# Performance work log

Measured on AMD Instinct MI355X. Metric: run time of the kernel, lower is better.

## Reference

```python
import jax, jax.numpy as jnp
import numpy as np

NUM_HEADS = 8
LN_EPS = 1e-5


def _layernorm(t, w, b):
    mu = t.mean(-1, keepdims=True)
    var = t.var(-1, keepdims=True)  # ddof=0, matches torch LayerNorm
    return (t - mu) * jax.lax.rsqrt(var + LN_EPS) * w + b


def setup_inputs() -> dict:
    key = jax.random.key(0)
    ks = jax.random.split(key, 5)
    B, C, H, W = 16, 384, 32, 32
    hidden = 4 * C
    s = 0.02
    return {
        "x": jax.random.normal(ks[0], (B, C, H, W), jnp.float32),
        "ln1_w": jnp.ones((C,), jnp.float32),
        "ln1_b": jnp.zeros((C,), jnp.float32),
        "qkv_w": s * jax.random.normal(ks[1], (3 * C, C), jnp.float32),
        "qkv_b": jnp.zeros((3 * C,), jnp.float32),
        "proj_w": s * jax.random.normal(ks[2], (C, C), jnp.float32),
        "proj_b": jnp.zeros((C,), jnp.float32),
        "ln2_w": jnp.ones((C,), jnp.float32),
        "ln2_b": jnp.zeros((C,), jnp.float32),
        "fc1_w": s * jax.random.normal(ks[3], (hidden, C), jnp.float32),
        "fc1_b": jnp.zeros((hidden,), jnp.float32),
        "fc2_w": s * jax.random.normal(ks[4], (C, hidden), jnp.float32),
        "fc2_b": jnp.zeros((C,), jnp.float32),
    }


def reference(x, ln1_w, ln1_b, qkv_w, qkv_b, proj_w, proj_b,
              ln2_w, ln2_b, fc1_w, fc1_b, fc2_w, fc2_b):
    B, C, H, W = x.shape
    N = H * W
    nh = NUM_HEADS
    hd = C // nh
    scale = hd ** (-0.5)

    xf = x.reshape(B, C, N).transpose(0, 2, 1)  # (B, N, C) tokens

    # --- pre-norm attention ---
    h1 = _layernorm(xf, ln1_w, ln1_b)
    qkv = h1 @ qkv_w.T + qkv_b                      # (B, N, 3C)
    qkv = qkv.reshape(B, N, 3, nh, hd).transpose(2, 0, 3, 1, 4)  # (3,B,h,N,d)
    q, k, v = qkv[0], qkv[1], qkv[2]
    attn = jax.nn.softmax(jnp.einsum('bhnd,bhmd->bhnm', q, k) * scale, axis=-1)
    out = jnp.einsum('bhnm,bhmd->bhnd', attn, v)    # (B,h,N,d)
    out = out.transpose(0, 2, 1, 3).reshape(B, N, C)
    out = out @ proj_w.T + proj_b
    xf = xf + out

    # --- pre-norm FFN (exact GELU, matching torch nn.GELU default) ---
    h2 = _layernorm(xf, ln2_w, ln2_b)
    f = jax.nn.gelu(h2 @ fc1_w.T + fc1_b, approximate=False)
    f = f @ fc2_w.T + fc2_b
    xf = xf + f

    return xf.transpose(0, 2, 1).reshape(B, C, H, W)
```

## Files before the change

kernel.cpp:

```cpp
#include <hip/hip_runtime.h>

typedef unsigned short u16;
using bf16x8 = __attribute__((ext_vector_type(8))) short;
using f32x4  = __attribute__((ext_vector_type(4))) float;
using f32x16 = __attribute__((ext_vector_type(16))) float;

#define DEV __device__ __forceinline__

constexpr int    NTOK = 16384;
constexpr size_t QKSZ = (size_t)16 * 8 * 1024 * 64;
constexpr float  ATTN_SCALE = 0.14433756729740645f;

DEV u16 f2bf(float x) {
  unsigned int u = __float_as_uint(x);
  u += 0x7fffu + ((u >> 16) & 1u);
  return (u16)(u >> 16);
}

DEV void async16(const u16* g, u16* l) {
  __builtin_amdgcn_global_load_lds(
      (const __attribute__((address_space(1))) unsigned int*)g,
      (__attribute__((address_space(3))) unsigned int*)l, 16, 0, 0);
}

DEV const bf16x8* lds_swz(const u16* base, int row, int bytecol) {
  int byte = row * 128 + bytecol;
  byte ^= (row & 7) << 4;
  return (const bf16x8*)((const char*)base + byte);
}

DEV f32x16 zero16() {
  f32x16 z;
#pragma unroll
  for (int i = 0; i < 16; ++i) z[i] = 0.f;
  return z;
}

DEV float gelu_f(float x) {
  float y = 0.7978845608028654f * (x + 0.044715f * x * x * x);
  float e = __expf(2.f * y);
  float t = 1.f - 2.f / (e + 1.f);
  return 0.5f * x * (1.f + t);
}

DEV void xcd_remap(int& bx, int& by) {
  int p = blockIdx.x + gridDim.x * blockIdx.y;
  int nxs = gridDim.x >> 3;
  int xcd = p & 7, q = p >> 3;
  bx = xcd * nxs + q % nxs;
  by = q / nxs;
}

__global__ void cvt_kernel(const float* __restrict__ qkvw, const float* __restrict__ qkvb,
                           const float* __restrict__ projw, const float* __restrict__ fc1w,
                           const float* __restrict__ fc2w,
                           u16* __restrict__ wqkvp, float* __restrict__ biasp,
                           u16* __restrict__ wproj, u16* __restrict__ wfc1,
                           u16* __restrict__ wfc2) {
  int i = blockIdx.x * 256 + threadIdx.x;
  if (i < 147456) {
    int p = i / 96, q = (i - p * 96) * 4;
    int which = p >> 9, h = (p >> 6) & 7, d = p & 63;
    ushort4 o{0, 0, 0, 0};
    if (d < 48) {
      float sc = which ? 1.f : ATTN_SCALE;
      float4 v = *(const float4*)(qkvw + (size_t)(which * 384 + h * 48 + d) * 384 + q);
      o = ushort4{f2bf(v.x * sc), f2bf(v.y * sc), f2bf(v.z * sc), f2bf(v.w * sc)};
    }
    *(ushort4*)(wqkvp + (size_t)p * 384 + q) = o;
  } else if (i < 479232) {
    const float* s; u16* d; int off;
    if (i < 184320)      { s = projw; d = wproj; off = i - 147456; }
    else if (i < 331776) { s = fc1w;  d = wfc1;  off = i - 184320; }
    else                 { s = fc2w;  d = wfc2;  off = i - 331776; }
    float4 v = *(const float4*)(s + (size_t)off * 4);
    *(ushort4*)(d + (size_t)off * 4) = ushort4{f2bf(v.x), f2bf(v.y), f2bf(v.z), f2bf(v.w)};
  } else if (i < 479616) {
    int qi = (i - 479232) * 4;
    float4 o;
    float* op = (float*)&o;
#pragma unroll
    for (int r = 0; r < 4; ++r) {
      int p = qi + r, which = p >> 9, h = (p >> 6) & 7, d = p & 63;
      op[r] = (d < 48) ? qkvb[which * 384 + h * 48 + d] * (which ? 1.f : ATTN_SCALE) : 0.f;
    }
    *(float4*)(biasp + qi) = o;
  }
}

__global__ __launch_bounds__(256) void ln_kernel(
    const float* __restrict__ in, const float* __restrict__ gw,
    const float* __restrict__ gb, u16* __restrict__ out) {
  __shared__ float tile[32][385];
  __shared__ float mu_s[32], rs_s[32];
  const int b = blockIdx.y;
  const int n0 = blockIdx.x * 32;
  const int t = threadIdx.x;
  const int j = t & 31, cb = t >> 5;
  const float* src = in + (size_t)b * 384 * 1024 + n0;
  for (int k = 0; k < 48; ++k) {
    int c = k * 8 + cb;
    tile[j][c] = src[(size_t)c * 1024 + j];
  }
  __syncthreads();
  const int jt = t >> 3, r = t & 7;
  float s = 0.f, ss = 0.f;
  for (int c = r; c < 384; c += 8) { float v = tile[jt][c]; s += v; ss += v * v; }
  s += __shfl_xor(s, 1); ss += __shfl_xor(ss, 1);
  s += __shfl_xor(s, 2); ss += __shfl_xor(ss, 2);
  s += __shfl_xor(s, 4); ss += __shfl_xor(ss, 4);
  const float mean = s * (1.f / 384.f);
  const float var  = ss * (1.f / 384.f) - mean * mean;
  if (r == 0) { mu_s[jt] = mean; rs_s[jt] = rsqrtf(var + 1e-5f); }
  __syncthreads();
  for (int q = t; q < 3072; q += 256) {
    int tok = q / 96, c4 = (q - tok * 96) * 4;
    float m = mu_s[tok], rv = rs_s[tok];
    float4 wv = *(const float4*)(gw + c4);
    float4 bv = *(const float4*)(gb + c4);
    u16* dst = out + (size_t)(b * 1024 + n0 + tok) * 384 + c4;
    ushort4 o{f2bf((tile[tok][c4 + 0] - m) * rv * wv.x + bv.x),
              f2bf((tile[tok][c4 + 1] - m) * rv * wv.y + bv.y),
              f2bf((tile[tok][c4 + 2] - m) * rv * wv.z + bv.z),
              f2bf((tile[tok][c4 + 3] - m) * rv * wv.w + bv.w)};
    *(ushort4*)dst = o;
  }
}

template<int EPI>
__global__ __launch_bounds__(256, 4) void gemm_kernel(
    const u16* __restrict__ A, const u16* __restrict__ W,
    const float* __restrict__ bias, float* __restrict__ outf,
    u16* __restrict__ outh, const float* __restrict__ resid, int K) {
  constexpr bool SWAP = (EPI == 1 || EPI == 3 || EPI == 4);
  __shared__ u16 sA[2][4096], sB[2][4096];
  int bx, by; xcd_remap(bx, by);
  const int m0 = bx * 128;
  const int n0 = (EPI == 4 ? 1024 : 0) + by * 128;
  const int wv = threadIdx.x >> 6, lane = threadIdx.x & 63;
  const int wm = (wv >> 1) * 64, wn = (wv & 1) * 64;
  const int l16 = lane & 15, lg = lane >> 4;
  const int rsw = (lg ^ (l16 & 3)) << 4;

  f32x4 acc[4][4];
#pragma unroll
  for (int i = 0; i < 4; ++i)
#pragma unroll
    for (int jj = 0; jj < 4; ++jj) acc[i][jj] = f32x4{0.f, 0.f, 0.f, 0.f};

  const int nk = K >> 5;
  auto stage = [&](int buf, int kt) {
    const u16* Ab = A + (size_t)m0 * K + kt * 32;
    const u16* Wb = W + (size_t)n0 * K + kt * 32;
#pragma unroll
    for (int i = 0; i < 2; ++i) {
      int cb = i * 256 + wv * 64;
      int c = cb + lane;
      int row = c >> 2, sl = (c & 3) ^ (row & 3);
      async16(Ab + (size_t)row * K + sl * 8, &sA[buf][cb * 8]);
      async16(Wb + (size_t)row * K + sl * 8, &sB[buf][cb * 8]);
    }
  };
  stage(0, 0);
  int buf = 0;
  for (int kt = 0; kt < nk; ++kt) {
    asm volatile("s_waitcnt vmcnt(0)" ::: "memory");
    __builtin_amdgcn_s_barrier();
    if (kt + 1 < nk) stage(buf ^ 1, kt + 1);
    bf16x8 av[4], bv[4];
#pragma unroll
    for (int f = 0; f < 4; ++f) {
      av[f] = *(const bf16x8*)((const char*)&sA[buf][0] + (wm + f * 16 + l16) * 64 + rsw);
      bv[f] = *(const bf16x8*)((const char*)&sB[buf][0] + (wn + f * 16 + l16) * 64 + rsw);
    }
    __builtin_amdgcn_s_setprio(1);
#pragma unroll
    for (int mf = 0; mf < 4; ++mf)
#pragma unroll
      for (int nf = 0; nf < 4; ++nf) {
        if constexpr (SWAP)
          acc[mf][nf] = __builtin_amdgcn_mfma_f32_16x16x32_bf16(bv[nf], av[mf], acc[mf][nf], 0, 0, 0);
        else
          acc[mf][nf] = __builtin_amdgcn_mfma_f32_16x16x32_bf16(av[mf], bv[nf], acc[mf][nf], 0, 0, 0);
      }
    __builtin_amdgcn_s_setprio(0);
    buf ^= 1;
  }

  if constexpr (!SWAP) {
#pragma unroll
    for (int mf = 0; mf < 4; ++mf) {
      const int mm = m0 + wm + mf * 16 + lg * 4;
      const int b = mm >> 10, nnb = mm & 1023;
#pragma unroll
      for (int nf = 0; nf < 4; ++nf) {
        const int col = n0 + wn + nf * 16 + l16;
        f32x4 v = acc[mf][nf];
        const float bs = bias[col];
        if constexpr (EPI == 0) {
          const int which = col >> 9, h = (col >> 6) & 7, d0 = col & 63;
          size_t base = (size_t)which * QKSZ + (((size_t)(b * 8 + h)) << 16) + (size_t)nnb * 64 + d0;
#pragma unroll
          for (int rr = 0; rr < 4; ++rr) outh[base + (size_t)rr * 64] = f2bf(v[rr] + bs);
        } else {
#pragma unroll
          for (int rr = 0; rr < 4; ++rr)
            outh[(size_t)(mm + rr) * 1536 + col] = f2bf(gelu_f(v[rr] + bs));
        }
      }
    }
  } else {
#pragma unroll
    for (int mf = 0; mf < 4; ++mf) {
      const int token = m0 + wm + mf * 16 + l16;
      const int b = token >> 10, nn = token & 1023;
#pragma unroll
      for (int nf = 0; nf < 4; ++nf) {
        const int colb = n0 + wn + nf * 16 + lg * 4;
        f32x4 v = acc[mf][nf];
        float4 bb = *(const float4*)(bias + colb);
        if constexpr (EPI == 4) {
#pragma unroll
          for (int rr = 0; rr < 4; ++rr) {
            const int col = colb + rr, h = (col >> 6) & 7, d = col & 63;
            outh[2ull * QKSZ + (((size_t)((b * 8 + h) * 64 + d)) << 10) + nn] =
                f2bf(v[rr] + ((const float*)&bb)[rr]);
          }
        } else {
#pragma unroll
          for (int rr = 0; rr < 4; ++rr) {
            const int col = colb + rr;
            size_t idx = (((size_t)(b * 384 + col)) << 10) + nn;
            outf[idx] = v[rr] + ((const float*)&bb)[rr] + resid[idx];
          }
        }
      }
    }
  }
}

__global__ __launch_bounds__(256, 3) void attn_kernel(
    const u16* __restrict__ Qg, const u16* __restrict__ Kg,
    const u16* __restrict__ Vtg, u16* __restrict__ outp) {
  __shared__ u16 Ks[2][4096];
  __shared__ u16 Vs[2][4096];
  __shared__ u16 Qs[8192];
  const int orig = blockIdx.x;
  const int swz = (orig & 7) * 128 + (orig >> 3);
  const int bh = swz >> 3, qt = swz & 7;
  const int w = threadIdx.x >> 6, lane = threadIdx.x & 63;
  const int l31 = lane & 31, hi = lane >> 5;

  const u16* kbase = Kg + (size_t)bh * 65536;
  const u16* vbase = Vtg + (size_t)bh * 65536;

  auto stageKV = [&](int buf, int kv) {
#pragma unroll
    for (int i = 0; i < 2; ++i) {
      int cb = (i * 4 + w) * 64;
      int ck = cb + lane;
      int g  = ck ^ ((ck >> 3) & 7);
      async16(kbase + (size_t)kv * 4096 + g * 8, &Ks[buf][cb * 8]);
      async16(vbase + (size_t)(g >> 3) * 1024 + kv * 64 + (g & 7) * 8, &Vs[buf][cb * 8]);
    }
  };

  {
    const u16* src = Qg + (size_t)(bh * 1024 + qt * 128) * 64;
#pragma unroll
    for (int i = 0; i < 4; ++i) {
      int cb = (i * 4 + w) * 64;
      int ck = cb + lane;
      int g  = ck ^ ((ck >> 3) & 7);
      async16(src + g * 8, &Qs[cb * 8]);
    }
  }
  stageKV(0, 0);
  asm volatile("s_waitcnt vmcnt(0)" ::: "memory");
  __builtin_amdgcn_s_barrier();

  bf16x8 qf[4];
#pragma unroll
  for (int ds = 0; ds < 4; ++ds)
    qf[ds] = *lds_swz(Qs, w * 32 + l31, ds * 32 + hi * 16);

  f32x16 out0 = zero16(), out1 = zero16();
  float ls0 = 0.f, ls1 = 0.f;

  int buf = 0;
  for (int kv = 0; kv < 16; ++kv) {
    if (kv + 1 < 16) stageKV(buf ^ 1, kv + 1);

    f32x16 sacc0 = zero16(), sacc1 = zero16();
    __builtin_amdgcn_s_setprio(1);
#pragma unroll
    for (int ds = 0; ds < 4; ++ds) {
      bf16x8 kf0 = *lds_swz(Ks[buf], l31,      ds * 32 + hi * 16);
      bf16x8 kf1 = *lds_swz(Ks[buf], 32 + l31, ds * 32 + hi * 16);
      sacc0 = __builtin_amdgcn_mfma_f32_32x32x16_bf16(kf0, qf[ds], sacc0, 0, 0, 0);
      sacc1 = __builtin_amdgcn_mfma_f32_32x32x16_bf16(kf1, qf[ds], sacc1, 0, 0, 0);
    }
    __builtin_amdgcn_s_setprio(0);

    unsigned int c0[8], c1[8];
#pragma unroll
    for (int i = 0; i < 8; ++i) {
      float a = __expf(sacc0[2 * i]), b = __expf(sacc0[2 * i + 1]);
      ls0 += a + b;
      unsigned int pk;
      asm("v_cvt_pk_bf16_f32 %0, %1, %2" : "=v"(pk) : "v"(a), "v"(b));
      c0[i] = pk;
    }
#pragma unroll
    for (int i = 0; i < 8; ++i) {
      float a = __expf(sacc1[2 * i]), b = __expf(sacc1[2 * i + 1]);
      ls1 += a + b;
      unsigned int pk;
      asm("v_cvt_pk_bf16_f32 %0, %1, %2" : "=v"(pk) : "v"(a), "v"(b));
      c1[i] = pk;
    }

#pragma unroll
    for (int m = 0; m < 4; ++m) {
      unsigned int a0 = (m < 2) ? c0[(m & 1) * 4 + 0] : c1[(m & 1) * 4 + 0];
      unsigned int b0 = (m < 2) ? c0[(m & 1) * 4 + 2] : c1[(m & 1) * 4 + 2];
      unsigned int a1 = (m < 2) ? c0[(m & 1) * 4 + 1] : c1[(m & 1) * 4 + 1];
      unsigned int b1 = (m < 2) ? c0[(m & 1) * 4 + 3] : c1[(m & 1) * 4 + 3];
      asm volatile("v_permlane32_swap_b32 %0, %1" : "+v"(a0), "+v"(b0));
      asm volatile("v_permlane32_swap_b32 %0, %1" : "+v"(a1), "+v"(b1));
      union { int4 i; bf16x8 v; } u;
      u.i = int4{(int)a0, (int)a1, (int)b0, (int)b1};
      bf16x8 pa = u.v;
      bf16x8 v0 = *lds_swz(Vs[buf], l31,      m * 32 + hi * 16);
      bf16x8 v1 = *lds_swz(Vs[buf], 32 + l31, m * 32 + hi * 16);
      __builtin_amdgcn_s_setprio(1);
      out0 = __builtin_amdgcn_mfma_f32_32x32x16_bf16(pa, v0, out0, 0, 0, 0);
      out1 = __builtin_amdgcn_mfma_f32_32x32x16_bf16(pa, v1, out1, 0, 0, 0);
      __builtin_amdgcn_s_setprio(0);
    }

    asm volatile("s_waitcnt vmcnt(0)" ::: "memory");
    __builtin_amdgcn_s_barrier();
    buf ^= 1;
  }

  float lf = ls0 + ls1;
  lf += __shfl_xor(lf, 32);
  const int b = bh >> 3, h = bh & 7;
#pragma unroll
  for (int r = 0; r < 16; ++r) {
    const int q = (r & 3) + 8 * (r >> 2) + 4 * hi;
    const float inv = 1.f / __shfl(lf, q);
    const int token = qt * 128 + w * 32 + q;
    const size_t rowb = (size_t)(b * 1024 + token) * 384 + h * 48;
    outp[rowb + l31] = f2bf(out0[r] * inv);
    if (l31 < 16) outp[rowb + 32 + l31] = f2bf(out1[r] * inv);
  }
}

constexpr size_t OFF_WQKVP = 0;
constexpr size_t OFF_BIASP = 1179648;
constexpr size_t OFF_WPROJ = 1185792;
constexpr size_t OFF_WFC1  = 1480704;
constexpr size_t OFF_WFC2  = 2660352;
constexpr size_t OFF_H     = 3840000;
constexpr size_t OFF_QKV   = 16422912;
constexpr size_t OFF_AO    = 66754560;
constexpr size_t OFF_Y1T   = 79337472;

extern "C" void kernel_launch(void* const* d_in, const int* in_sizes, int n_in,
                              void* d_out, int out_size, void* d_ws, size_t ws_size,
                              hipStream_t stream) {
  (void)in_sizes; (void)n_in; (void)out_size; (void)ws_size;
  const float* x     = (const float*)d_in[0];
  const float* ln1w  = (const float*)d_in[1];
  const float* ln1b  = (const float*)d_in[2];
  const float* qkvw  = (const float*)d_in[3];
  const float* qkvbi = (const float*)d_in[4];
  const float* projw = (const float*)d_in[5];
  const float* projb = (const float*)d_in[6];
  const float* ln2w  = (const float*)d_in[7];
  const float* ln2b  = (const float*)d_in[8];
  const float* fc1w  = (const float*)d_in[9];
  const float* fc1b  = (const float*)d_in[10];
  const float* fc2w  = (const float*)d_in[11];
  const float* fc2b  = (const float*)d_in[12];

  char* ws = (char*)d_ws;
  u16*   wqkvp = (u16*)(ws + OFF_WQKVP);
  float* biasp = (float*)(ws + OFF_BIASP);
  u16*   wproj = (u16*)(ws + OFF_WPROJ);
  u16*   wfc1  = (u16*)(ws + OFF_WFC1);
  u16*   wfc2  = (u16*)(ws + OFF_WFC2);
  u16*   h1    = (u16*)(ws + OFF_H);
  u16*   qkvs  = (u16*)(ws + OFF_QKV);
  u16*   f1    = qkvs;
  u16*   ao    = (u16*)(ws + OFF_AO);
  float* y1t   = (float*)(ws + OFF_Y1T);

  cvt_kernel<<<1874, 256, 0, stream>>>(qkvw, qkvbi, projw, fc1w, fc2w,
                                       wqkvp, biasp, wproj, wfc1, wfc2);

  dim3 lngrid(32, 16);
  ln_kernel<<<lngrid, 256, 0, stream>>>(x, ln1w, ln1b, h1);

  gemm_kernel<0><<<dim3(128, 8), 256, 0, stream>>>(h1, wqkvp, biasp, nullptr, qkvs, nullptr, 384);
  gemm_kernel<4><<<dim3(128, 4), 256, 0, stream>>>(h1, wqkvp, biasp, nullptr, qkvs, nullptr, 384);

  attn_kernel<<<dim3(1024), 256, 0, stream>>>(qkvs, qkvs + QKSZ, qkvs + 2 * QKSZ, ao);

  gemm_kernel<1><<<dim3(128, 3), 256, 0, stream>>>(ao, wproj, projb, y1t, nullptr, x, 384);

  ln_kernel<<<lngrid, 256, 0, stream>>>(y1t, ln2w, ln2b, h1 );

  gemm_kernel<2><<<dim3(128, 12), 256, 0, stream>>>(h1, wfc1, fc1b, nullptr, f1, nullptr, 384);

  gemm_kernel<3><<<dim3(128, 3), 256, 0, stream>>>(f1, wfc2, fc2b, (float*)d_out, nullptr, y1t, 1536);
}
```

Before: 314.2 us.

## Triple-buffer GEMM and attention K/V loads, merge QKV GEMM launches

Both the GEMM and attention kernels go from double to triple buffering, keeping two tiles in flight and waiting with vmcnt(4) instead of draining all loads before each iteration. The attention kernel moves its barrier to the top of the loop and reuses the Q staging region for the third K/V buffer. The two QKV GEMM launches (Q/K row-major and transposed V) become one launch, with the output layout chosen per block at runtime. The costs are more shared memory per block, which lowers the GEMM occupancy hint from 4 to 3, and a runtime branch on the MFMA operand order.

```diff
diff --git a/kernel.cpp b/kernel.cpp
--- a/kernel.cpp
+++ b/kernel.cpp
@@ -128,15 +128,21 @@
 }
 
 template<int EPI>
-__global__ __launch_bounds__(256, 4) void gemm_kernel(
+__global__ __launch_bounds__(256, 3) void gemm_kernel(
     const u16* __restrict__ A, const u16* __restrict__ W,
     const float* __restrict__ bias, float* __restrict__ outf,
     u16* __restrict__ outh, const float* __restrict__ resid, int K) {
-  constexpr bool SWAP = (EPI == 1 || EPI == 3 || EPI == 4);
-  __shared__ u16 sA[2][4096], sB[2][4096];
+  __shared__ u16 sA[3][4096], sB[3][4096];
   int bx, by; xcd_remap(bx, by);
   const int m0 = bx * 128;
-  const int n0 = (EPI == 4 ? 1024 : 0) + by * 128;
+  bool swp; int n0;
+  if constexpr (EPI == 5) {
+    swp = (by >= 8);
+    n0 = swp ? 1024 + (by - 8) * 128 : by * 128;
+  } else {
+    swp = (EPI == 1 || EPI == 3 || EPI == 4);
+    n0 = (EPI == 4 ? 1024 : 0) + by * 128;
+  }
   const int wv = threadIdx.x >> 6, lane = threadIdx.x & 63;
   const int wm = (wv >> 1) * 64, wn = (wv & 1) * 64;
   const int l16 = lane & 15, lg = lane >> 4;
@@ -162,11 +168,13 @@
     }
   };
   stage(0, 0);
+  stage(1, 1);
   int buf = 0;
   for (int kt = 0; kt < nk; ++kt) {
-    asm volatile("s_waitcnt vmcnt(0)" ::: "memory");
+    if (kt < nk - 1) asm volatile("s_waitcnt vmcnt(4)" ::: "memory");
+    else             asm volatile("s_waitcnt vmcnt(0)" ::: "memory");
     __builtin_amdgcn_s_barrier();
-    if (kt + 1 < nk) stage(buf ^ 1, kt + 1);
+    if (kt + 2 < nk) { int nb = buf + 2; if (nb >= 3) nb -= 3; stage(nb, kt + 2); }
     bf16x8 av[4], bv[4];
 #pragma unroll
     for (int f = 0; f < 4; ++f) {
@@ -174,20 +182,24 @@
       bv[f] = *(const bf16x8*)((const char*)&sB[buf][0] + (wn + f * 16 + l16) * 64 + rsw);
     }
     __builtin_amdgcn_s_setprio(1);
-#pragma unroll
-    for (int mf = 0; mf < 4; ++mf)
-#pragma unroll
-      for (int nf = 0; nf < 4; ++nf) {
-        if constexpr (SWAP)
+    if (!swp) {
+#pragma unroll
+      for (int mf = 0; mf < 4; ++mf)
+#pragma unroll
+        for (int nf = 0; nf < 4; ++nf)
+          acc[mf][nf] = __builtin_amdgcn_mfma_f32_16x16x32_bf16(av[mf], bv[nf], acc[mf][nf], 0, 0, 0);
+    } else {
+#pragma unroll
+      for (int mf = 0; mf < 4; ++mf)
+#pragma unroll
+        for (int nf = 0; nf < 4; ++nf)
           acc[mf][nf] = __builtin_amdgcn_mfma_f32_16x16x32_bf16(bv[nf], av[mf], acc[mf][nf], 0, 0, 0);
-        else
-          acc[mf][nf] = __builtin_amdgcn_mfma_f32_16x16x32_bf16(av[mf], bv[nf], acc[mf][nf], 0, 0, 0);
-      }
+    }
     __builtin_amdgcn_s_setprio(0);
-    buf ^= 1;
-  }
-
-  if constexpr (!SWAP) {
+    ++buf; if (buf >= 3) buf = 0;
+  }
+
+  if (!swp) {
 #pragma unroll
     for (int mf = 0; mf < 4; ++mf) {
       const int mm = m0 + wm + mf * 16 + lg * 4;
@@ -197,7 +209,7 @@
         const int col = n0 + wn + nf * 16 + l16;
         f32x4 v = acc[mf][nf];
         const float bs = bias[col];
-        if constexpr (EPI == 0) {
+        if constexpr (EPI == 0 || EPI == 5) {
           const int which = col >> 9, h = (col >> 6) & 7, d0 = col & 63;
           size_t base = (size_t)which * QKSZ + (((size_t)(b * 8 + h)) << 16) + (size_t)nnb * 64 + d0;
 #pragma unroll
@@ -219,7 +231,7 @@
         const int colb = n0 + wn + nf * 16 + lg * 4;
         f32x4 v = acc[mf][nf];
         float4 bb = *(const float4*)(bias + colb);
-        if constexpr (EPI == 4) {
+        if constexpr (EPI == 4 || EPI == 5) {
 #pragma unroll
           for (int rr = 0; rr < 4; ++rr) {
             const int col = colb + rr, h = (col >> 6) & 7, d = col & 63;
@@ -242,9 +254,8 @@
 __global__ __launch_bounds__(256, 3) void attn_kernel(
     const u16* __restrict__ Qg, const u16* __restrict__ Kg,
     const u16* __restrict__ Vtg, u16* __restrict__ outp) {
-  __shared__ u16 Ks[2][4096];
-  __shared__ u16 Vs[2][4096];
-  __shared__ u16 Qs[8192];
+  __shared__ u16 lds[24576];
+  u16* const Qs = lds + 4096;
   const int orig = blockIdx.x;
   const int swz = (orig & 7) * 128 + (orig >> 3);
   const int bh = swz >> 3, qt = swz & 7;
@@ -260,8 +271,9 @@
       int cb = (i * 4 + w) * 64;
       int ck = cb + lane;
       int g  = ck ^ ((ck >> 3) & 7);
-      async16(kbase + (size_t)kv * 4096 + g * 8, &Ks[buf][cb * 8]);
-      async16(vbase + (size_t)(g >> 3) * 1024 + kv * 64 + (g & 7) * 8, &Vs[buf][cb * 8]);
+      async16(kbase + (size_t)kv * 4096 + g * 8, &lds[buf * 4096 + cb * 8]);
+      async16(vbase + (size_t)(g >> 3) * 1024 + kv * 64 + (g & 7) * 8,
+              &lds[12288 + buf * 4096 + cb * 8]);
     }
   };
 
@@ -276,27 +288,35 @@
     }
   }
   stageKV(0, 0);
-  asm volatile("s_waitcnt vmcnt(0)" ::: "memory");
+  asm volatile("s_waitcnt vmcnt(4)" ::: "memory");
   __builtin_amdgcn_s_barrier();
 
   bf16x8 qf[4];
 #pragma unroll
   for (int ds = 0; ds < 4; ++ds)
     qf[ds] = *lds_swz(Qs, w * 32 + l31, ds * 32 + hi * 16);
+  asm volatile("s_waitcnt lgkmcnt(0)" ::: "memory");
+  __builtin_amdgcn_s_barrier();
+  stageKV(1, 1);
 
   f32x16 out0 = zero16(), out1 = zero16();
   float ls0 = 0.f, ls1 = 0.f;
 
   int buf = 0;
   for (int kv = 0; kv < 16; ++kv) {
-    if (kv + 1 < 16) stageKV(buf ^ 1, kv + 1);
+    if (kv < 15) asm volatile("s_waitcnt vmcnt(4)" ::: "memory");
+    else         asm volatile("s_waitcnt vmcnt(0)" ::: "memory");
+    __builtin_amdgcn_s_barrier();
+    if (kv + 2 < 16) { int nb = buf + 2; if (nb >= 3) nb -= 3; stageKV(nb, kv + 2); }
+    const u16* Kb = &lds[buf * 4096];
+    const u16* Vb = &lds[12288 + buf * 4096];
 
     f32x16 sacc0 = zero16(), sacc1 = zero16();
     __builtin_amdgcn_s_setprio(1);
 #pragma unroll
     for (int ds = 0; ds < 4; ++ds) {
-      bf16x8 kf0 = *lds_swz(Ks[buf], l31,      ds * 32 + hi * 16);
-      bf16x8 kf1 = *lds_swz(Ks[buf], 32 + l31, ds * 32 + hi * 16);
+      bf16x8 kf0 = *lds_swz(Kb, l31,      ds * 32 + hi * 16);
+      bf16x8 kf1 = *lds_swz(Kb, 32 + l31, ds * 32 + hi * 16);
       sacc0 = __builtin_amdgcn_mfma_f32_32x32x16_bf16(kf0, qf[ds], sacc0, 0, 0, 0);
       sacc1 = __builtin_amdgcn_mfma_f32_32x32x16_bf16(kf1, qf[ds], sacc1, 0, 0, 0);
     }
@@ -326,22 +346,19 @@
       unsigned int b0 = (m < 2) ? c0[(m & 1) * 4 + 2] : c1[(m & 1) * 4 + 2];
       unsigned int a1 = (m < 2) ? c0[(m & 1) * 4 + 1] : c1[(m & 1) * 4 + 1];
       unsigned int b1 = (m < 2) ? c0[(m & 1) * 4 + 3] : c1[(m & 1) * 4 + 3];
-      asm volatile("v_permlane32_swap_b32 %0, %1" : "+v"(a0), "+v"(b0));
-      asm volatile("v_permlane32_swap_b32 %0, %1" : "+v"(a1), "+v"(b1));
+      asm("v_permlane32_swap_b32 %0, %1" : "+v"(a0), "+v"(b0));
+      asm("v_permlane32_swap_b32 %0, %1" : "+v"(a1), "+v"(b1));
       union { int4 i; bf16x8 v; } u;
       u.i = int4{(int)a0, (int)a1, (int)b0, (int)b1};
       bf16x8 pa = u.v;
-      bf16x8 v0 = *lds_swz(Vs[buf], l31,      m * 32 + hi * 16);
-      bf16x8 v1 = *lds_swz(Vs[buf], 32 + l31, m * 32 + hi * 16);
+      bf16x8 v0 = *lds_swz(Vb, l31,      m * 32 + hi * 16);
+      bf16x8 v1 = *lds_swz(Vb, 32 + l31, m * 32 + hi * 16);
       __builtin_amdgcn_s_setprio(1);
       out0 = __builtin_amdgcn_mfma_f32_32x32x16_bf16(pa, v0, out0, 0, 0, 0);
       out1 = __builtin_amdgcn_mfma_f32_32x32x16_bf16(pa, v1, out1, 0, 0, 0);
       __builtin_amdgcn_s_setprio(0);
     }
-
-    asm volatile("s_waitcnt vmcnt(0)" ::: "memory");
-    __builtin_amdgcn_s_barrier();
-    buf ^= 1;
+    ++buf; if (buf >= 3) buf = 0;
   }
 
   float lf = ls0 + ls1;
@@ -404,8 +421,7 @@
   dim3 lngrid(32, 16);
   ln_kernel<<<lngrid, 256, 0, stream>>>(x, ln1w, ln1b, h1);
 
-  gemm_kernel<0><<<dim3(128, 8), 256, 0, stream>>>(h1, wqkvp, biasp, nullptr, qkvs, nullptr, 384);
-  gemm_kernel<4><<<dim3(128, 4), 256, 0, stream>>>(h1, wqkvp, biasp, nullptr, qkvs, nullptr, 384);
+  gemm_kernel<5><<<dim3(128, 12), 256, 0, stream>>>(h1, wqkvp, biasp, nullptr, qkvs, nullptr, 384);
 
   attn_kernel<<<dim3(1024), 256, 0, stream>>>(qkvs, qkvs + QKSZ, qkvs + 2 * QKSZ, ao);
 
```

Result: no change. 316.4 us (+0.7%).
